# Performance work log

Measured on AMD Instinct MI355X. Metric: run time of the kernel, lower is better.

## Reference

```python
import jax, jax.numpy as jnp
import numpy as np

EPS = 1e-5


def _in_relu(y):
    # instance norm (no affine, biased var, eps=1e-5) + ReLU, y: [B,C,H,W]
    mu = jnp.mean(y, axis=(-2, -1), keepdims=True)
    var = jnp.mean((y - mu) ** 2, axis=(-2, -1), keepdims=True)
    return jax.nn.relu((y - mu) * jax.lax.rsqrt(var + EPS))


def _conv3(x, w, b):
    # x: [C,H,W], w: [O,I,3,3] -> [O,H,W]
    y = jax.lax.conv_general_dilated(x[None], w, (1, 1), ((1, 1), (1, 1)),
                                     dimension_numbers=('NCHW', 'OIHW', 'NCHW'))[0]
    return y + b[:, None, None]


def _mod_block(x, W, b, mod):
    # per-sample weight modulation: mod[n] * W, then conv+IN+relu; x: [B,C,H,W], mod: [B,O,I,3,3]
    y = jax.vmap(lambda xi, mi: _conv3(xi, mi * W, b))(x, mod)
    return _in_relu(y)


def _maxpool2(x):
    return jax.lax.reduce_window(x, -jnp.inf, jax.lax.max, (1, 1, 2, 2), (1, 1, 2, 2), 'VALID')


def _up2(x):
    B, C, H, W = x.shape
    # bilinear, half-pixel centers == PyTorch align_corners=False
    return jax.image.resize(x, (B, C, 2 * H, 2 * W), method='bilinear')


def _conv1x1(x, w, b):
    y = jax.lax.conv_general_dilated(x, w, (1, 1), 'VALID',
                                     dimension_numbers=('NCHW', 'OIHW', 'NCHW'))
    return y + b[None, :, None, None]


def setup_inputs() -> dict:
    key = jax.random.key(0)
    B, H, W = 8, 256, 256
    ks = iter(jax.random.split(key, 64))
    d = {}
    d['us_query_input'] = jax.random.normal(next(ks), (B, 1, H, W), jnp.float32)
    d['ksp_query_imgs'] = jax.random.normal(next(ks), (B, H, W, 2), jnp.float32)
    d['ksp_mask_query'] = jax.random.uniform(next(ks), (B, H, W), jnp.float32)
    down_io = [(1, 32), (32, 64), (64, 128), (128, 256)]
    up_io = [(512, 128), (256, 64), (128, 32), (64, 32)]
    for i, (ci, co) in enumerate(down_io):
        d[f'down_mod_{i}'] = jax.random.normal(next(ks), (B, co, ci, 3, 3), jnp.float32)
        d[f'W_d{i}'] = 0.05 * jax.random.normal(next(ks), (co, ci, 3, 3), jnp.float32)
        d[f'b_d{i}'] = 0.05 * jax.random.normal(next(ks), (co,), jnp.float32)
    d['latent_mod'] = jax.random.normal(next(ks), (B, 256, 256, 3, 3), jnp.float32)
    d['W_lat'] = 0.05 * jax.random.normal(next(ks), (256, 256, 3, 3), jnp.float32)
    d['b_lat'] = 0.05 * jax.random.normal(next(ks), (256,), jnp.float32)
    for i, (ci, co) in enumerate(up_io):
        d[f'up_mod_{i}'] = jax.random.normal(next(ks), (B, co, ci, 3, 3), jnp.float32)
        d[f'W_u{i}'] = 0.05 * jax.random.normal(next(ks), (co, ci, 3, 3), jnp.float32)
        d[f'b_u{i}'] = 0.05 * jax.random.normal(next(ks), (co,), jnp.float32)
    d['w_c1'] = 0.05 * jax.random.normal(next(ks), (16, 32, 1, 1), jnp.float32)
    d['b_c1'] = 0.05 * jax.random.normal(next(ks), (16,), jnp.float32)
    d['w_c2'] = 0.05 * jax.random.normal(next(ks), (1, 16, 1, 1), jnp.float32)
    d['b_c2'] = 0.05 * jax.random.normal(next(ks), (1,), jnp.float32)
    d['w_c3'] = 0.05 * jax.random.normal(next(ks), (1, 1, 1, 1), jnp.float32)
    d['b_c3'] = 0.05 * jax.random.normal(next(ks), (1,), jnp.float32)
    return d


def reference(us_query_input, ksp_query_imgs, ksp_mask_query,
              down_mod_0, down_mod_1, down_mod_2, down_mod_3,
              latent_mod, up_mod_0, up_mod_1, up_mod_2, up_mod_3,
              W_d0, b_d0, W_d1, b_d1, W_d2, b_d2, W_d3, b_d3,
              W_lat, b_lat,
              W_u0, b_u0, W_u1, b_u1, W_u2, b_u2, W_u3, b_u3,
              w_c1, b_c1, w_c2, b_c2, w_c3, b_c3):
    x0 = us_query_input
    out = x0
    skips = []
    downs = [(W_d0, b_d0, down_mod_0), (W_d1, b_d1, down_mod_1),
             (W_d2, b_d2, down_mod_2), (W_d3, b_d3, down_mod_3)]
    for Wc, bc, m in downs:
        out = _mod_block(out, Wc, bc, m)
        skips.append(out)
        out = _maxpool2(out)
    out = _mod_block(out, W_lat, b_lat, latent_mod)
    ups = [(W_u0, b_u0, up_mod_0), (W_u1, b_u1, up_mod_1),
           (W_u2, b_u2, up_mod_2), (W_u3, b_u3, up_mod_3)]
    for Wc, bc, m in ups:
        out = _up2(out)
        out = jnp.concatenate([out, skips.pop()], axis=1)
        out = _mod_block(out, Wc, bc, m)
    out = _conv1x1(_conv1x1(_conv1x1(out, w_c1, b_c1), w_c2, b_c2), w_c3, b_c3)
    out = out + x0
    # FFT data consistency
    pred = out[:, 0]                                  # [B,H,W]
    kpred = jnp.fft.fft2(pred, norm='ortho')
    ksp = ksp_query_imgs[..., 0] + 1j * ksp_query_imgs[..., 1]
    upd = ksp_mask_query * ksp + (1.0 - ksp_mask_query) * kpred
    img = jnp.fft.ifft2(upd, norm='ortho')
    return jnp.real(img)[:, None].astype(jnp.float32)   # [B,1,H,W]
```

## Files before the change

kernel.cpp:

```cpp
#include <hip/hip_runtime.h>


#define EPS_IN 1e-5f
constexpr int STST = 7936;

typedef __attribute__((ext_vector_type(8))) short short8;
typedef __attribute__((ext_vector_type(4))) short short4_t;
typedef __attribute__((ext_vector_type(4))) float f32x4;

__device__ __forceinline__ short f2bf(float f) {
    unsigned u = __float_as_uint(f);
    unsigned r = (u + 0x7fffu + ((u >> 16) & 1u)) >> 16;
    return (short)r;
}
__device__ __forceinline__ float bf2f(short s) {
    return __uint_as_float(((unsigned)(unsigned short)s) << 16);
}

__global__ void zero_f(float* __restrict__ p, int n)
{
    int i = blockIdx.x * 256 + threadIdx.x;
    if (i < n) p[i] = 0.f;
}

struct WmJobs {
    const float* W[8];
    const float* mod[8];
    short* wm[8];
    int Co[8];
    int Ci[8];
    int cum[9];
};

__global__ void make_wm_all(WmJobs j)
{
    int idx = blockIdx.x * 256 + threadIdx.x;
    if (idx >= j.cum[8]) return;
    int l = 0;
    while (idx >= j.cum[l + 1]) ++l;
    int local = idx - j.cum[l];
    const int Ci = j.Ci[l], Co = j.Co[l];
    int ci = local % Ci;
    int rem = local / Ci;
    int co = rem % Co;
    int b = rem / Co;
    const float* wp = j.W[l] + (size_t)(co * Ci + ci) * 9;
    const float* mp = j.mod[l] + ((size_t)((size_t)b * Co + co) * Ci + ci) * 9;
    short* wm = j.wm[l];
#pragma unroll
    for (int k = 0; k < 9; ++k)
        wm[(((size_t)(b * 9 + k) * Co + co) * Ci + ci)] = f2bf(wp[k] * mp[k]);
}

template <int VR, int NCOG, bool UP>
__global__ __launch_bounds__(256) void conv3x3_cl(
    const short* __restrict__ x1, int Ci1,
    const short* __restrict__ x2,
    const float2* __restrict__ st1, float invHW1,
    const short* __restrict__ wm,
    short* __restrict__ y,
    float2* __restrict__ stats,
    int Ci, int Co, int H, int W)
{
    constexpr int TH = 4 * VR, SH = TH + 2, SW = 18;
    constexpr int STN = UP ? 256 : 1;
    constexpr bool DW = (TH * 16 * NCOG * 16 * 2) <= (SH * SW * 32 * 2);
    __shared__ __align__(16) short s_x[SH][SW][32];
    __shared__ float s_red[4][4][NCOG][4][2];
    __shared__ float2 s_st1[STN];

    const int tid = threadIdx.x;
    const int lane = tid & 63, wv = tid >> 6;
    const int m = lane & 15, g = lane >> 4;

    const int b = blockIdx.x & 7;
    int r = blockIdx.x >> 3;
    const int nCoB = Co / (16 * NCOG);
    const int coblk = r % nCoB;
    const int tileId = r / nCoB;
    const int tilesx = W >> 4;
    const int tx0 = (tileId % tilesx) * 16;
    const int ty0 = (tileId / tilesx) * TH;
    const int co0 = coblk * (16 * NCOG);
    const int Ci2 = Ci - Ci1;
    const int Hs = H >> 1, Ws = W >> 1;
    const int bucket = tileId & 7;

    if (UP) {
        for (int i = tid; i < Ci1; i += 256) {
            float sx = 0.f, sy = 0.f;
#pragma unroll
            for (int k = 0; k < 8; ++k) {
                float2 v = st1[(size_t)k * STST + (size_t)b * Ci1 + i];
                sx += v.x; sy += v.y;
            }
            float mu = sx * invHW1;
            float var = sy * invHW1 - mu * mu;
            s_st1[i] = make_float2(mu, rsqrtf(var + EPS_IN));
        }
    }

    f32x4 acc[NCOG][VR];
#pragma unroll
    for (int cg = 0; cg < NCOG; ++cg)
#pragma unroll
        for (int rr = 0; rr < VR; ++rr) acc[cg][rr] = (f32x4)0.f;

    const short* wmb = wm + (size_t)b * 9 * Co * Ci;
    const short* x1b = x1 + (size_t)b * (UP ? (size_t)Hs * Ws : (size_t)H * W) * Ci1;
    const short* x2b = x2 + (size_t)b * H * W * Ci2;

    for (int ci0 = 0; ci0 < Ci; ci0 += 32) {
        __syncthreads();
        if (UP && ci0 < Ci1) {
            const int cb = ci0;
            for (int idx = tid; idx < SH * SW * 4; idx += 256) {
                int gg = idx & 3, pos = idx >> 2;
                int yy = pos / SW, xx = pos - yy * SW;
                int gy = ty0 + yy - 1, gx = tx0 + xx - 1;
                short8 v = (short8)0;
                if (gy >= 0 && gy < H && gx >= 0 && gx < W) {
                    int xk = gx >> 1, yk = gy >> 1;
                    int xo = gx & 1, yo = gy & 1;
                    int xa = xo ? xk : (xk > 0 ? xk - 1 : 0);
                    int xb = xo ? (xk + 1 < Ws ? xk + 1 : Ws - 1) : xk;
                    float wxa = xo ? 0.75f : 0.25f;
                    int ya = yo ? yk : (yk > 0 ? yk - 1 : 0);
                    int yb = yo ? (yk + 1 < Hs ? yk + 1 : Hs - 1) : yk;
                    float wya = yo ? 0.75f : 0.25f;
                    const short* ib = x1b + cb + gg * 8;
                    short8 vaa = *(const short8*)(ib + ((size_t)ya * Ws + xa) * Ci1);
                    short8 vab = *(const short8*)(ib + ((size_t)ya * Ws + xb) * Ci1);
                    short8 vba = *(const short8*)(ib + ((size_t)yb * Ws + xa) * Ci1);
                    short8 vbb = *(const short8*)(ib + ((size_t)yb * Ws + xb) * Ci1);
#pragma unroll
                    for (int e = 0; e < 8; ++e) {
                        float2 sv = s_st1[cb + gg * 8 + e];
                        float aa = fmaxf(0.f, (bf2f(vaa[e]) - sv.x) * sv.y);
                        float ab = fmaxf(0.f, (bf2f(vab[e]) - sv.x) * sv.y);
                        float ba = fmaxf(0.f, (bf2f(vba[e]) - sv.x) * sv.y);
                        float bb = fmaxf(0.f, (bf2f(vbb[e]) - sv.x) * sv.y);
                        float r0 = wxa * aa + (1.f - wxa) * ab;
                        float r1 = wxa * ba + (1.f - wxa) * bb;
                        v[e] = f2bf(wya * r0 + (1.f - wya) * r1);
                    }
                }
                *(short8*)&s_x[yy][xx][(gg ^ (xx & 3)) * 8] = v;
            }
        } else {
            const short* src; int C, cb;
            if (ci0 < Ci1) { src = x1b; C = Ci1; cb = ci0; }
            else           { src = x2b; C = Ci2; cb = ci0 - Ci1; }
            for (int idx = tid; idx < SH * SW * 4; idx += 256) {
                int gg = idx & 3, pos = idx >> 2;
                int yy = pos / SW, xx = pos - yy * SW;
                int gy = ty0 + yy - 1, gx = tx0 + xx - 1;
                short8 v = (short8)0;
                if (gy >= 0 && gy < H && gx >= 0 && gx < W)
                    v = *(const short8*)(src + ((size_t)gy * W + gx) * C + cb + gg * 8);
                *(short8*)&s_x[yy][xx][(gg ^ (xx & 3)) * 8] = v;
            }
        }
        __syncthreads();
#pragma unroll
        for (int t = 0; t < 9; ++t) {
            const int dy = t / 3, dx = t - 3 * (t / 3);
            const short* wr = wmb + ((size_t)t * Co + co0) * Ci + ci0 + g * 8;
            short8 a[NCOG];
#pragma unroll
            for (int cg = 0; cg < NCOG; ++cg)
                a[cg] = *(const short8*)(wr + (size_t)(cg * 16 + m) * Ci);
            const int xx = m + dx;
            const int sgo = (g ^ (xx & 3)) * 8;
#pragma unroll
            for (int rr = 0; rr < VR; ++rr) {
                short8 bf = *(const short8*)&s_x[wv * VR + rr + dy][xx][sgo];
#pragma unroll
                for (int cg = 0; cg < NCOG; ++cg)
                    acc[cg][rr] = __builtin_amdgcn_mfma_f32_16x16x32_bf16(a[cg], bf, acc[cg][rr], 0, 0, 0);
            }
        }
    }

    if constexpr (DW) {
        __syncthreads();
        short* sd = (short*)&s_x[0][0][0];
#pragma unroll
        for (int cg = 0; cg < NCOG; ++cg)
#pragma unroll
            for (int rr = 0; rr < VR; ++rr) {
                short4_t o;
#pragma unroll
                for (int q = 0; q < 4; ++q) o[q] = f2bf(acc[cg][rr][q]);
                *(short4_t*)&sd[((wv * VR + rr) * 16 + m) * (NCOG * 16) + cg * 16 + g * 4] = o;
            }
        __syncthreads();
        constexpr int N16 = TH * 16 * NCOG * 2;
        constexpr int CPR = NCOG * 32;
        for (int c = tid; c < N16; c += 256) {
            int row = c / CPR;
            int o16 = c % CPR;
            int p = o16 / (NCOG * 2);
            int cw = o16 % (NCOG * 2);
            short8 v = *(short8*)&sd[(row * 16 + p) * (NCOG * 16) + cw * 8];
            *(short8*)(y + (((size_t)b * H + ty0 + row) * W + tx0 + p) * Co + co0 + cw * 8) = v;
        }
    } else {
        const int ox = tx0 + m;
#pragma unroll
        for (int cg = 0; cg < NCOG; ++cg)
#pragma unroll
            for (int rr = 0; rr < VR; ++rr) {
                int oy = ty0 + wv * VR + rr;
                short4_t o;
#pragma unroll
                for (int q = 0; q < 4; ++q) o[q] = f2bf(acc[cg][rr][q]);
                *(short4_t*)(y + (((size_t)b * H + oy) * W + ox) * Co + co0 + cg * 16 + g * 4) = o;
            }
    }

#pragma unroll
    for (int cg = 0; cg < NCOG; ++cg)
#pragma unroll
        for (int q = 0; q < 4; ++q) {
            float s = 0.f, s2 = 0.f;
#pragma unroll
            for (int rr = 0; rr < VR; ++rr) { float v = acc[cg][rr][q]; s += v; s2 += v * v; }
#pragma unroll
            for (int msk = 1; msk < 16; msk <<= 1) { s += __shfl_xor(s, msk); s2 += __shfl_xor(s2, msk); }
            if (m == 0) { s_red[wv][g][cg][q][0] = s; s_red[wv][g][cg][q][1] = s2; }
        }
    __syncthreads();
    for (int i = tid; i < 16 * NCOG; i += 256) {
        int q = i & 3, gg = (i >> 2) & 3, cg = i >> 4;
        float S = 0.f, S2 = 0.f;
#pragma unroll
        for (int w = 0; w < 4; ++w) { S += s_red[w][gg][cg][q][0]; S2 += s_red[w][gg][cg][q][1]; }
        float* sp = (float*)&stats[(size_t)bucket * STST + (size_t)b * Co + co0 + i];
        atomicAdd(sp, S); atomicAdd(sp + 1, S2);
    }
}

__global__ __launch_bounds__(256) void conv_d0_cl(
    const float* __restrict__ x0, const float* __restrict__ W,
    const float* __restrict__ mod, short* __restrict__ y,
    float2* __restrict__ stats)
{
    __shared__ float s[18][18];
    __shared__ float sw[32][9];
    __shared__ float s_red[8][32][2];
    __shared__ __align__(16) short sd[16][16][32];
    const int tid = threadIdx.x;
    const int tx = tid & 15, ty = tid >> 4;
    const int tx0 = (blockIdx.x & 15) * 16, ty0 = (blockIdx.x >> 4) * 16;
    const int b = blockIdx.y;
    if (tid < 288) sw[tid / 9][tid % 9] = W[tid] * mod[b * 288 + tid];
    for (int pos = tid; pos < 18 * 18; pos += 256) {
        int yy = pos / 18, xx = pos - yy * 18;
        int gy = ty0 + yy - 1, gx = tx0 + xx - 1;
        bool inb = gy >= 0 && gy < 256 && gx >= 0 && gx < 256;
        s[yy][xx] = inb ? x0[((size_t)b << 16) + gy * 256 + gx] : 0.f;
    }
    __syncthreads();
    float v[3][3];
#pragma unroll
    for (int r = 0; r < 3; ++r)
#pragma unroll
        for (int c = 0; c < 3; ++c) v[r][c] = s[ty + r][tx + c];
    float vals[32];
#pragma unroll
    for (int co = 0; co < 32; ++co) {
        float a = 0.f;
#pragma unroll
        for (int r = 0; r < 3; ++r)
#pragma unroll
            for (int c = 0; c < 3; ++c) a = fmaf(v[r][c], sw[co][r * 3 + c], a);
        vals[co] = a;
    }
#pragma unroll
    for (int j = 0; j < 4; ++j) {
        short8 o;
#pragma unroll
        for (int e = 0; e < 8; ++e) o[e] = f2bf(vals[j * 8 + e]);
        *(short8*)&sd[ty][tx][j * 8] = o;
    }
    __syncthreads();
    for (int c = tid; c < 1024; c += 256) {
        int row = c >> 6, o = c & 63;
        short8 vv = *(short8*)&sd[row][o >> 2][(o & 3) * 8];
        *(short8*)(y + (((size_t)b * 256 + ty0 + row) * 256 + tx0 + (o >> 2)) * 32 + (o & 3) * 8) = vv;
    }
    {
        const int c = tid & 31, grp = tid >> 5;
        const short* sdf = (const short*)sd;
        float ss = 0.f, ss2 = 0.f;
#pragma unroll
        for (int p = 0; p < 32; ++p) {
            float vv = bf2f(sdf[(grp * 32 + p) * 32 + c]);
            ss += vv; ss2 += vv * vv;
        }
        s_red[grp][c][0] = ss;
        s_red[grp][c][1] = ss2;
    }
    __syncthreads();
    if (tid < 32) {
        float S = 0.f, S2 = 0.f;
#pragma unroll
        for (int g2 = 0; g2 < 8; ++g2) { S += s_red[g2][tid][0]; S2 += s_red[g2][tid][1]; }
        int bucket = blockIdx.x & 7;
        float* sp = (float*)&stats[(size_t)bucket * STST + (size_t)b * 32 + tid];
        atomicAdd(sp, S); atomicAdd(sp + 1, S2);
    }
}

__global__ __launch_bounds__(256) void maxpool_cl(
    short* __restrict__ in, const float2* __restrict__ st, float invHW,
    short* __restrict__ out, int c8s, int ws, int hs, int total8)
{
    const int C = 8 << c8s;
    __shared__ float2 sst[2048];
    for (int i = threadIdx.x; i < 8 * C; i += 256) {
        int bb = i / C, c = i % C;
        float sx = 0.f, sy = 0.f;
#pragma unroll
        for (int k = 0; k < 8; ++k) {
            float2 v = st[(size_t)k * STST + (size_t)bb * C + c];
            sx += v.x; sy += v.y;
        }
        float mu = sx * invHW;
        sst[i] = make_float2(mu, rsqrtf(sy * invHW - mu * mu + EPS_IN));
    }
    __syncthreads();
    for (int idx = blockIdx.x * 256 + threadIdx.x; idx < total8; idx += gridDim.x * 256) {
        int c8 = idx & ((1 << c8s) - 1);
        int p = idx >> c8s;
        int x = p & ((1 << ws) - 1);
        int yy = (p >> ws) & ((1 << hs) - 1);
        int b = p >> (ws + hs);
        short* ip = in + (((size_t)b * (2 << hs) + 2 * yy) * (2 << ws) + 2 * x) * C + c8 * 8;
        size_t rs = (size_t)(2 << ws) * C;
        short8 v0 = *(const short8*)ip, v1 = *(const short8*)(ip + C);
        short8 v2 = *(const short8*)(ip + rs), v3 = *(const short8*)(ip + rs + C);
        short8 o, w0, w1, w2, w3;
#pragma unroll
        for (int e = 0; e < 8; ++e) {
            float2 sv = sst[b * C + c8 * 8 + e];
            float n0 = fmaxf(0.f, (bf2f(v0[e]) - sv.x) * sv.y);
            float n1 = fmaxf(0.f, (bf2f(v1[e]) - sv.x) * sv.y);
            float n2 = fmaxf(0.f, (bf2f(v2[e]) - sv.x) * sv.y);
            float n3 = fmaxf(0.f, (bf2f(v3[e]) - sv.x) * sv.y);
            w0[e] = f2bf(n0); w1[e] = f2bf(n1); w2[e] = f2bf(n2); w3[e] = f2bf(n3);
            o[e] = f2bf(fmaxf(fmaxf(n0, n1), fmaxf(n2, n3)));
        }
        *(short8*)ip = w0;
        *(short8*)(ip + C) = w1;
        *(short8*)(ip + rs) = w2;
        *(short8*)(ip + rs + C) = w3;
        *(short8*)(out + (size_t)idx * 8) = o;
    }
}

__global__ __launch_bounds__(256) void upsample_cl(
    const short* __restrict__ in, const float2* __restrict__ st, float invHW,
    short* __restrict__ out, int c8s, int wsi, int hsi, int total8)
{
    const int C = 8 << c8s;
    const int Win = 1 << wsi, Hin = 1 << hsi;
    __shared__ float2 sst[2048];
    for (int i = threadIdx.x; i < 8 * C; i += 256) {
        int bb = i / C, c = i % C;
        float sx = 0.f, sy = 0.f;
#pragma unroll
        for (int k = 0; k < 8; ++k) {
            float2 v = st[(size_t)k * STST + (size_t)bb * C + c];
            sx += v.x; sy += v.y;
        }
        float mu = sx * invHW;
        sst[i] = make_float2(mu, rsqrtf(sy * invHW - mu * mu + EPS_IN));
    }
    __syncthreads();
    for (int idx = blockIdx.x * 256 + threadIdx.x; idx < total8; idx += gridDim.x * 256) {
        int c8 = idx & ((1 << c8s) - 1);
        int p = idx >> c8s;
        int x = p & (2 * Win - 1);
        int yy = (p >> (wsi + 1)) & (2 * Hin - 1);
        int b = p >> (wsi + 1 + hsi + 1);
        int xk = x >> 1, yk = yy >> 1;
        int xa, xb; float wxa;
        if (x & 1) { xa = xk; xb = (xk + 1 < Win) ? xk + 1 : Win - 1; wxa = 0.75f; }
        else       { xa = (xk > 0) ? xk - 1 : 0; xb = xk; wxa = 0.25f; }
        int ya, yb; float wya;
        if (yy & 1) { ya = yk; yb = (yk + 1 < Hin) ? yk + 1 : Hin - 1; wya = 0.75f; }
        else        { ya = (yk > 0) ? yk - 1 : 0; yb = yk; wya = 0.25f; }
        const short* ib = in + (size_t)b * Hin * Win * C + c8 * 8;
        short8 vaa = *(const short8*)(ib + ((size_t)ya * Win + xa) * C);
        short8 vab = *(const short8*)(ib + ((size_t)ya * Win + xb) * C);
        short8 vba = *(const short8*)(ib + ((size_t)yb * Win + xa) * C);
        short8 vbb = *(const short8*)(ib + ((size_t)yb * Win + xb) * C);
        short8 o;
#pragma unroll
        for (int e = 0; e < 8; ++e) {
            float2 sv = sst[b * C + c8 * 8 + e];
            float aa = fmaxf(0.f, (bf2f(vaa[e]) - sv.x) * sv.y);
            float ab = fmaxf(0.f, (bf2f(vab[e]) - sv.x) * sv.y);
            float ba = fmaxf(0.f, (bf2f(vba[e]) - sv.x) * sv.y);
            float bb = fmaxf(0.f, (bf2f(vbb[e]) - sv.x) * sv.y);
            float r0 = wxa * aa + (1.f - wxa) * ab;
            float r1 = wxa * ba + (1.f - wxa) * bb;
            o[e] = f2bf(wya * r0 + (1.f - wya) * r1);
        }
        *(short8*)(out + (size_t)idx * 8) = o;
    }
}

__global__ void eff1x1(const float* __restrict__ w1, const float* __restrict__ b1,
                       const float* __restrict__ w2, const float* __restrict__ b2,
                       const float* __restrict__ w3, const float* __restrict__ b3,
                       float* __restrict__ eff)
{
    int t = threadIdx.x;
    if (t < 32) {
        float s = 0.f;
        for (int k = 0; k < 16; ++k) s += w2[k] * w1[k * 32 + t];
        eff[t] = w3[0] * s;
    }
    if (t == 32) {
        float s = 0.f;
        for (int k = 0; k < 16; ++k) s += w2[k] * b1[k];
        eff[32] = w3[0] * (s + b2[0]) + b3[0];
    }
}

__device__ __forceinline__ void fft256(float2* s, int tid, float sign)
{
    __syncthreads();
#pragma unroll
    for (int t = 0; t < 4; ++t) {
        int i = tid + t * 64;
        int r = __brev(i) >> 24;
        if (r > i) { float2 tmp = s[i]; s[i] = s[r]; s[r] = tmp; }
    }
    __syncthreads();
    for (int st = 1; st <= 8; ++st) {
        int m = 1 << st, half = m >> 1;
#pragma unroll
        for (int t = 0; t < 2; ++t) {
            int k = tid + t * 64;
            int g = k >> (st - 1), j = k & (half - 1);
            int i0 = (g << st) + j, i1 = i0 + half;
            float ang = sign * 6.283185307179586f * (float)j / (float)m;
            float sn, cs;
            __sincosf(ang, &sn, &cs);
            float2 a = s[i0], b = s[i1];
            float2 tt = make_float2(b.x * cs - b.y * sn, b.x * sn + b.y * cs);
            s[i0] = make_float2(a.x + tt.x, a.y + tt.y);
            s[i1] = make_float2(a.x - tt.x, a.y - tt.y);
        }
        __syncthreads();
    }
}

__global__ __launch_bounds__(64) void final_fft_rows(
    const short* __restrict__ act, const float2* __restrict__ st, float invHW,
    const float* __restrict__ x0, const float* __restrict__ eff,
    float2* __restrict__ cplx)
{
    __shared__ float2 s[256];
    __shared__ float2 sst[32];
    __shared__ float seff[33];
    const int row = blockIdx.x, tid = threadIdx.x;
    const int b = row >> 8, yy = row & 255;
    if (tid < 32) {
        float sx = 0.f, sy = 0.f;
#pragma unroll
        for (int k = 0; k < 8; ++k) {
            float2 v = st[(size_t)k * STST + (size_t)b * 32 + tid];
            sx += v.x; sy += v.y;
        }
        float mu = sx * invHW;
        sst[tid] = make_float2(mu, rsqrtf(sy * invHW - mu * mu + EPS_IN));
    }
    if (tid < 33) seff[tid] = eff[tid];
    __syncthreads();
#pragma unroll
    for (int k = 0; k < 4; ++k) {
        int x = k * 64 + tid;
        const short8* a = (const short8*)(act + (((size_t)b * 256 + yy) * 256 + x) * 32);
        float sacc = seff[32] + x0[((size_t)b << 16) + (yy << 8) + x];
#pragma unroll
        for (int j = 0; j < 4; ++j) {
            short8 v = a[j];
#pragma unroll
            for (int e = 0; e < 8; ++e) {
                float2 sv = sst[j * 8 + e];
                sacc += seff[j * 8 + e] * fmaxf(0.f, (bf2f(v[e]) - sv.x) * sv.y);
            }
        }
        s[x] = make_float2(sacc, 0.f);
    }
    fft256(s, tid, -1.f);
    float2* o = cplx + (size_t)row * 256;
    for (int i = tid; i < 256; i += 64) o[i] = s[i];
}

__global__ __launch_bounds__(64) void fft_cols_combine(float2* __restrict__ data,
                                                       const float* __restrict__ ksp,
                                                       const float* __restrict__ mask)
{
    __shared__ float2 s[256];
    int col = blockIdx.x & 255, b = blockIdx.x >> 8;
    int tid = threadIdx.x;
    float2* base = data + (size_t)b * 65536 + col;
    for (int i = tid; i < 256; i += 64) s[i] = base[(size_t)i * 256];
    fft256(s, tid, -1.f);
    for (int i = tid; i < 256; i += 64) {
        size_t mi = ((size_t)b * 256 + i) * 256 + col;
        float m = mask[mi];
        float2 kp = s[i];
        float kr = ksp[mi * 2], ki = ksp[mi * 2 + 1];
        s[i] = make_float2(m * kr + (1.f - m) * kp.x * (1.f / 256.f),
                           m * ki + (1.f - m) * kp.y * (1.f / 256.f));
    }
    fft256(s, tid, 1.f);
    for (int i = tid; i < 256; i += 64) base[(size_t)i * 256] = s[i];
}

__global__ __launch_bounds__(64) void fft_rows_inv(const float2* __restrict__ data,
                                                   float* __restrict__ out)
{
    __shared__ float2 s[256];
    int row = blockIdx.x, tid = threadIdx.x;
    const float2* p = data + (size_t)row * 256;
    for (int i = tid; i < 256; i += 64) s[i] = p[i];
    fft256(s, tid, 1.f);
    float* o = out + (size_t)row * 256;
    for (int i = tid; i < 256; i += 64) o[i] = s[i].x * (1.f / 256.f);
}

extern "C" void kernel_launch(void* const* d_in, const int* in_sizes, int n_in,
                              void* d_out, int out_size, void* d_ws, size_t ws_size,
                              hipStream_t stream)
{
    (void)in_sizes; (void)n_in; (void)out_size; (void)ws_size;

    const float* x0 = (const float*)d_in[0];
    const float* ksp = (const float*)d_in[1];
    const float* mask = (const float*)d_in[2];
    const float* mod_d[4] = {(const float*)d_in[3], (const float*)d_in[6],
                             (const float*)d_in[9], (const float*)d_in[12]};
    const float* W_d[4] = {(const float*)d_in[4], (const float*)d_in[7],
                           (const float*)d_in[10], (const float*)d_in[13]};
    const float* mod_lat = (const float*)d_in[15];
    const float* W_lat = (const float*)d_in[16];
    const float* mod_u[4] = {(const float*)d_in[18], (const float*)d_in[21],
                             (const float*)d_in[24], (const float*)d_in[27]};
    const float* W_u[4] = {(const float*)d_in[19], (const float*)d_in[22],
                           (const float*)d_in[25], (const float*)d_in[28]};
    const float* w_c1 = (const float*)d_in[30];
    const float* b_c1 = (const float*)d_in[31];
    const float* w_c2 = (const float*)d_in[32];
    const float* b_c2 = (const float*)d_in[33];
    const float* w_c3 = (const float*)d_in[34];
    const float* b_c3 = (const float*)d_in[35];

    short* sA  = (short*)d_ws;
    short* sB  = sA + 16777216;
    short* sk0 = sB + 16777216;
    short* sk1 = sk0 + 16777216;
    short* sk2 = sk1 + 8388608;
    short* sk3 = sk2 + 4194304;
    short* wm_d1 = sk3 + 2097152;
    short* wm_d2 = wm_d1 + 147456;
    short* wm_d3 = wm_d2 + 589824;
    short* wm_lat = wm_d3 + 2359296;
    short* wm_u0 = wm_lat + 4718592;
    short* wm_u1 = wm_u0 + 4718592;
    short* wm_u2 = wm_u1 + 1179648;
    short* wm_u3 = wm_u2 + 294912;
    float2* cplx = (float2*)(wm_u3 + 147456);
    float2* stA = cplx + 524288;
    float* eff = (float*)(stA + 8 * STST);

    float2* st_d0 = stA + 0;
    float2* st_d1 = stA + 256;
    float2* st_d2 = stA + 768;
    float2* st_d3 = stA + 1792;
    float2* st_lat = stA + 3840;
    float2* st_u0 = stA + 5888;
    float2* st_u1 = stA + 6912;
    float2* st_u2 = stA + 7424;
    float2* st_u3 = stA + 7680;

    const float i64k = 1.f / 65536.f, i16k = 1.f / 16384.f, i4k = 1.f / 4096.f,
                i1k = 1.f / 1024.f, i256 = 1.f / 256.f;

    dim3 blk(256);

    zero_f<<<496, blk, 0, stream>>>((float*)stA, 8 * STST * 2);
    eff1x1<<<1, 64, 0, stream>>>(w_c1, b_c1, w_c2, b_c2, w_c3, b_c3, eff);

    WmJobs jobs;
    const float* Wl[8]  = {W_d[1], W_d[2], W_d[3], W_lat, W_u[0], W_u[1], W_u[2], W_u[3]};
    const float* Ml[8]  = {mod_d[1], mod_d[2], mod_d[3], mod_lat, mod_u[0], mod_u[1], mod_u[2], mod_u[3]};
    short* WMl[8] = {wm_d1, wm_d2, wm_d3, wm_lat, wm_u0, wm_u1, wm_u2, wm_u3};
    int Col[8] = {64, 128, 256, 256, 128, 64, 32, 32};
    int Cil[8] = {32, 64, 128, 256, 512, 256, 128, 64};
    jobs.cum[0] = 0;
    for (int l = 0; l < 8; ++l) {
        jobs.W[l] = Wl[l]; jobs.mod[l] = Ml[l]; jobs.wm[l] = WMl[l];
        jobs.Co[l] = Col[l]; jobs.Ci[l] = Cil[l];
        jobs.cum[l + 1] = jobs.cum[l] + 8 * Col[l] * Cil[l];
    }
    make_wm_all<<<(jobs.cum[8] + 255) / 256, blk, 0, stream>>>(jobs);

    conv_d0_cl<<<dim3(256, 8), blk, 0, stream>>>(x0, W_d[0], mod_d[0], sk0, st_d0);
    maxpool_cl<<<2048, blk, 0, stream>>>(sk0, st_d0, i64k, sA, 2, 7, 7, 524288);

    conv3x3_cl<4, 4, false><<<512, blk, 0, stream>>>(sA, 32, sA, stA, 0.f, wm_d1, sk1, st_d1, 32, 64, 128, 128);
    maxpool_cl<<<1024, blk, 0, stream>>>(sk1, st_d1, i16k, sA, 3, 6, 6, 262144);

    conv3x3_cl<2, 4, false><<<512, blk, 0, stream>>>(sA, 64, sA, stA, 0.f, wm_d2, sk2, st_d2, 64, 128, 64, 64);
    maxpool_cl<<<512, blk, 0, stream>>>(sk2, st_d2, i4k, sA, 4, 5, 5, 131072);

    conv3x3_cl<2, 2, false><<<512, blk, 0, stream>>>(sA, 128, sA, stA, 0.f, wm_d3, sk3, st_d3, 128, 256, 32, 32);
    maxpool_cl<<<256, blk, 0, stream>>>(sk3, st_d3, i1k, sA, 5, 4, 4, 65536);

    conv3x3_cl<2, 1, false><<<256, blk, 0, stream>>>(sA, 256, sA, stA, 0.f, wm_lat, sB, st_lat, 256, 256, 16, 16);

    upsample_cl<<<1024, blk, 0, stream>>>(sB, st_lat, i256, sA, 5, 4, 4, 262144);
    conv3x3_cl<2, 1, false><<<512, blk, 0, stream>>>(sA, 256, sk3, stA, 0.f, wm_u0, sB, st_u0, 512, 128, 32, 32);
    conv3x3_cl<2, 2, true><<<512, blk, 0, stream>>>(sB, 128, sk2, st_u0, i1k, wm_u1, sA, st_u1, 256, 64, 64, 64);
    conv3x3_cl<4, 2, true><<<512, blk, 0, stream>>>(sA, 64, sk1, st_u1, i4k, wm_u2, sB, st_u2, 128, 32, 128, 128);
    conv3x3_cl<4, 2, true><<<2048, blk, 0, stream>>>(sB, 32, sk0, st_u2, i16k, wm_u3, sA, st_u3, 64, 32, 256, 256);

    final_fft_rows<<<2048, 64, 0, stream>>>(sA, st_u3, i64k, x0, eff, cplx);

    fft_cols_combine<<<2048, 64, 0, stream>>>(cplx, ksp, mask);
    fft_rows_inv<<<2048, 64, 0, stream>>>(cplx, (float*)d_out);
}
```

Measured before the change: 471.3 us.

## Merge setup kernels, stage low-res normalized tile in LDS, batch column FFTs

Three setup launches (zeroing the stats buffer, building the effective 1x1 weights, building the modulated weights) become one kernel that branches on block index. The upsampling conv paths now load each low-resolution input tile once into shared memory with instance norm and ReLU already applied, so the bilinear gather no longer does four global loads and four normalizations per output pixel. The column FFT plus data-consistency step now processes 8 columns per 256-thread block with coalesced row loads, replacing the single-column 64-thread blocks that read with a 256-element stride. The trade is more shared memory and extra syncs in the conv, plus per-butterfly __sincosf twiddles in the new FFT.

```diff
diff --git a/kernel.cpp b/kernel.cpp
--- a/kernel.cpp
+++ b/kernel.cpp
@@ -17,39 +17,55 @@
     return __uint_as_float(((unsigned)(unsigned short)s) << 16);
 }
 
-__global__ void zero_f(float* __restrict__ p, int n)
-{
-    int i = blockIdx.x * 256 + threadIdx.x;
-    if (i < n) p[i] = 0.f;
-}
-
-struct WmJobs {
+struct SetupJobs {
     const float* W[8];
     const float* mod[8];
     short* wm[8];
     int Co[8];
     int Ci[8];
     int cum[9];
+    const float *w1, *b1, *w2, *b2, *w3, *b3;
+    float* eff;
+    float* stats;
+    int statN;
+    int wmBlocks;
 };
 
-__global__ void make_wm_all(WmJobs j)
-{
-    int idx = blockIdx.x * 256 + threadIdx.x;
-    if (idx >= j.cum[8]) return;
-    int l = 0;
-    while (idx >= j.cum[l + 1]) ++l;
-    int local = idx - j.cum[l];
-    const int Ci = j.Ci[l], Co = j.Co[l];
-    int ci = local % Ci;
-    int rem = local / Ci;
-    int co = rem % Co;
-    int b = rem / Co;
-    const float* wp = j.W[l] + (size_t)(co * Ci + ci) * 9;
-    const float* mp = j.mod[l] + ((size_t)((size_t)b * Co + co) * Ci + ci) * 9;
-    short* wm = j.wm[l];
-#pragma unroll
-    for (int k = 0; k < 9; ++k)
-        wm[(((size_t)(b * 9 + k) * Co + co) * Ci + ci)] = f2bf(wp[k] * mp[k]);
+__global__ void setup_all(SetupJobs j)
+{
+    const int bx = blockIdx.x, tid = threadIdx.x;
+    if (bx < j.wmBlocks) {
+        int idx = bx * 256 + tid;
+        if (idx >= j.cum[8]) return;
+        int l = 0;
+        while (idx >= j.cum[l + 1]) ++l;
+        int local = idx - j.cum[l];
+        const int Ci = j.Ci[l], Co = j.Co[l];
+        int ci = local % Ci;
+        int rem = local / Ci;
+        int co = rem % Co;
+        int b = rem / Co;
+        const float* wp = j.W[l] + (size_t)(co * Ci + ci) * 9;
+        const float* mp = j.mod[l] + ((size_t)((size_t)b * Co + co) * Ci + ci) * 9;
+        short* wm = j.wm[l];
+#pragma unroll
+        for (int k = 0; k < 9; ++k)
+            wm[(((size_t)(b * 9 + k) * Co + co) * Ci + ci)] = f2bf(wp[k] * mp[k]);
+    } else if (bx == j.wmBlocks) {
+        if (tid < 32) {
+            float s = 0.f;
+            for (int k = 0; k < 16; ++k) s += j.w2[k] * j.w1[k * 32 + tid];
+            j.eff[tid] = j.w3[0] * s;
+        }
+        if (tid == 32) {
+            float s = 0.f;
+            for (int k = 0; k < 16; ++k) s += j.w2[k] * j.b1[k];
+            j.eff[32] = j.w3[0] * (s + j.b2[0]) + j.b3[0];
+        }
+    } else {
+        int i = (bx - j.wmBlocks - 1) * 256 + tid;
+        if (i < j.statN) j.stats[i] = 0.f;
+    }
 }
 
 template <int VR, int NCOG, bool UP>
@@ -63,11 +79,14 @@
     int Ci, int Co, int H, int W)
 {
     constexpr int TH = 4 * VR, SH = TH + 2, SW = 18;
-    constexpr int STN = UP ? 256 : 1;
-    constexpr bool DW = (TH * 16 * NCOG * 16 * 2) <= (SH * SW * 32 * 2);
+    constexpr int STN = UP ? 128 : 1;
+    constexpr int LH = UP ? (TH / 2 + 2) : 1;
+    constexpr int LW = 10, LRW = LW * 8;
+    constexpr bool DW = (TH * 16 * NCOG * 16) <= (SH * SW * 32);
     __shared__ __align__(16) short s_x[SH][SW][32];
     __shared__ float s_red[4][4][NCOG][4][2];
     __shared__ float2 s_st1[STN];
+    __shared__ __align__(16) short s_lr[UP ? 4 : 1][LH][LRW];
 
     const int tid = threadIdx.x;
     const int lane = tid & 63, wv = tid >> 6;
@@ -114,6 +133,22 @@
         __syncthreads();
         if (UP && ci0 < Ci1) {
             const int cb = ci0;
+            const int ly0 = (ty0 >> 1) - 1, lx0 = (tx0 >> 1) - 1;
+            for (int i2 = tid; i2 < 4 * LH * LW; i2 += 256) {
+                int gg = i2 & 3, p2 = i2 >> 2;
+                int jj = p2 / LW, ii = p2 - jj * LW;
+                int sy2 = ly0 + jj; sy2 = sy2 < 0 ? 0 : (sy2 >= Hs ? Hs - 1 : sy2);
+                int sx2 = lx0 + ii; sx2 = sx2 < 0 ? 0 : (sx2 >= Ws ? Ws - 1 : sx2);
+                short8 v = *(const short8*)(x1b + ((size_t)sy2 * Ws + sx2) * Ci1 + cb + gg * 8);
+                short8 o;
+#pragma unroll
+                for (int e = 0; e < 8; ++e) {
+                    float2 sv = s_st1[cb + gg * 8 + e];
+                    o[e] = f2bf(fmaxf(0.f, (bf2f(v[e]) - sv.x) * sv.y));
+                }
+                *(short8*)&s_lr[gg][jj][ii * 8] = o;
+            }
+            __syncthreads();
             for (int idx = tid; idx < SH * SW * 4; idx += 256) {
                 int gg = idx & 3, pos = idx >> 2;
                 int yy = pos / SW, xx = pos - yy * SW;
@@ -128,20 +163,16 @@
                     int ya = yo ? yk : (yk > 0 ? yk - 1 : 0);
                     int yb = yo ? (yk + 1 < Hs ? yk + 1 : Hs - 1) : yk;
                     float wya = yo ? 0.75f : 0.25f;
-                    const short* ib = x1b + cb + gg * 8;
-                    short8 vaa = *(const short8*)(ib + ((size_t)ya * Ws + xa) * Ci1);
-                    short8 vab = *(const short8*)(ib + ((size_t)ya * Ws + xb) * Ci1);
-                    short8 vba = *(const short8*)(ib + ((size_t)yb * Ws + xa) * Ci1);
-                    short8 vbb = *(const short8*)(ib + ((size_t)yb * Ws + xb) * Ci1);
+                    int ja = ya - ly0, jb = yb - ly0;
+                    int ia = xa - lx0, ib2 = xb - lx0;
+                    short8 vaa = *(const short8*)&s_lr[gg][ja][ia * 8];
+                    short8 vab = *(const short8*)&s_lr[gg][ja][ib2 * 8];
+                    short8 vba = *(const short8*)&s_lr[gg][jb][ia * 8];
+                    short8 vbb = *(const short8*)&s_lr[gg][jb][ib2 * 8];
 #pragma unroll
                     for (int e = 0; e < 8; ++e) {
-                        float2 sv = s_st1[cb + gg * 8 + e];
-                        float aa = fmaxf(0.f, (bf2f(vaa[e]) - sv.x) * sv.y);
-                        float ab = fmaxf(0.f, (bf2f(vab[e]) - sv.x) * sv.y);
-                        float ba = fmaxf(0.f, (bf2f(vba[e]) - sv.x) * sv.y);
-                        float bb = fmaxf(0.f, (bf2f(vbb[e]) - sv.x) * sv.y);
-                        float r0 = wxa * aa + (1.f - wxa) * ab;
-                        float r1 = wxa * ba + (1.f - wxa) * bb;
+                        float r0 = wxa * bf2f(vaa[e]) + (1.f - wxa) * bf2f(vab[e]);
+                        float r1 = wxa * bf2f(vba[e]) + (1.f - wxa) * bf2f(vbb[e]);
                         v[e] = f2bf(wya * r0 + (1.f - wya) * r1);
                     }
                 }
@@ -413,24 +444,6 @@
     }
 }
 
-__global__ void eff1x1(const float* __restrict__ w1, const float* __restrict__ b1,
-                       const float* __restrict__ w2, const float* __restrict__ b2,
-                       const float* __restrict__ w3, const float* __restrict__ b3,
-                       float* __restrict__ eff)
-{
-    int t = threadIdx.x;
-    if (t < 32) {
-        float s = 0.f;
-        for (int k = 0; k < 16; ++k) s += w2[k] * w1[k * 32 + t];
-        eff[t] = w3[0] * s;
-    }
-    if (t == 32) {
-        float s = 0.f;
-        for (int k = 0; k < 16; ++k) s += w2[k] * b1[k];
-        eff[32] = w3[0] * (s + b2[0]) + b3[0];
-    }
-}
-
 __device__ __forceinline__ void fft256(float2* s, int tid, float sign)
 {
     __syncthreads();
@@ -503,26 +516,83 @@
     for (int i = tid; i < 256; i += 64) o[i] = s[i];
 }
 
-__global__ __launch_bounds__(64) void fft_cols_combine(float2* __restrict__ data,
-                                                       const float* __restrict__ ksp,
-                                                       const float* __restrict__ mask)
-{
-    __shared__ float2 s[256];
-    int col = blockIdx.x & 255, b = blockIdx.x >> 8;
-    int tid = threadIdx.x;
-    float2* base = data + (size_t)b * 65536 + col;
-    for (int i = tid; i < 256; i += 64) s[i] = base[(size_t)i * 256];
-    fft256(s, tid, -1.f);
-    for (int i = tid; i < 256; i += 64) {
-        size_t mi = ((size_t)b * 256 + i) * 256 + col;
-        float m = mask[mi];
-        float2 kp = s[i];
+__global__ __launch_bounds__(256) void fft_cols_combine8(
+    float2* __restrict__ data, const float* __restrict__ ksp,
+    const float* __restrict__ mask)
+{
+    __shared__ float2 s2[8][260];
+    const int tid = threadIdx.x;
+    const int b = blockIdx.x >> 5;
+    const int col0 = (blockIdx.x & 31) * 8;
+    float2* base = data + (size_t)b * 65536 + col0;
+    for (int idx = tid; idx < 2048; idx += 256) {
+        int row = idx >> 3, c = idx & 7;
+        s2[c][row] = base[row * 256 + c];
+    }
+    __syncthreads();
+    const int c = tid >> 5, lt = tid & 31;
+#pragma unroll
+    for (int t = 0; t < 8; ++t) {
+        int i = lt + t * 32;
+        int r = __brev(i) >> 24;
+        if (r > i) { float2 tmp = s2[c][i]; s2[c][i] = s2[c][r]; s2[c][r] = tmp; }
+    }
+    __syncthreads();
+    for (int st = 1; st <= 8; ++st) {
+        int m = 1 << st, half = m >> 1;
+#pragma unroll
+        for (int t = 0; t < 4; ++t) {
+            int k = lt + t * 32;
+            int g = k >> (st - 1), j = k & (half - 1);
+            int i0 = (g << st) + j, i1 = i0 + half;
+            float ang = -6.283185307179586f * (float)j / (float)m;
+            float sn, cs;
+            __sincosf(ang, &sn, &cs);
+            float2 a = s2[c][i0], bb = s2[c][i1];
+            float2 tt = make_float2(bb.x * cs - bb.y * sn, bb.x * sn + bb.y * cs);
+            s2[c][i0] = make_float2(a.x + tt.x, a.y + tt.y);
+            s2[c][i1] = make_float2(a.x - tt.x, a.y - tt.y);
+        }
+        __syncthreads();
+    }
+    for (int idx = tid; idx < 2048; idx += 256) {
+        int row = idx >> 3, cc = idx & 7;
+        size_t mi = ((size_t)b * 256 + row) * 256 + col0 + cc;
+        float mval = mask[mi];
+        float2 kp = s2[cc][row];
         float kr = ksp[mi * 2], ki = ksp[mi * 2 + 1];
-        s[i] = make_float2(m * kr + (1.f - m) * kp.x * (1.f / 256.f),
-                           m * ki + (1.f - m) * kp.y * (1.f / 256.f));
-    }
-    fft256(s, tid, 1.f);
-    for (int i = tid; i < 256; i += 64) base[(size_t)i * 256] = s[i];
+        s2[cc][row] = make_float2(mval * kr + (1.f - mval) * kp.x * (1.f / 256.f),
+                                  mval * ki + (1.f - mval) * kp.y * (1.f / 256.f));
+    }
+    __syncthreads();
+#pragma unroll
+    for (int t = 0; t < 8; ++t) {
+        int i = lt + t * 32;
+        int r = __brev(i) >> 24;
+        if (r > i) { float2 tmp = s2[c][i]; s2[c][i] = s2[c][r]; s2[c][r] = tmp; }
+    }
+    __syncthreads();
+    for (int st = 1; st <= 8; ++st) {
+        int m = 1 << st, half = m >> 1;
+#pragma unroll
+        for (int t = 0; t < 4; ++t) {
+            int k = lt + t * 32;
+            int g = k >> (st - 1), j = k & (half - 1);
+            int i0 = (g << st) + j, i1 = i0 + half;
+            float ang = 6.283185307179586f * (float)j / (float)m;
+            float sn, cs;
+            __sincosf(ang, &sn, &cs);
+            float2 a = s2[c][i0], bb = s2[c][i1];
+            float2 tt = make_float2(bb.x * cs - bb.y * sn, bb.x * sn + bb.y * cs);
+            s2[c][i0] = make_float2(a.x + tt.x, a.y + tt.y);
+            s2[c][i1] = make_float2(a.x - tt.x, a.y - tt.y);
+        }
+        __syncthreads();
+    }
+    for (int idx = tid; idx < 2048; idx += 256) {
+        int row = idx >> 3, cc = idx & 7;
+        base[row * 256 + cc] = s2[cc][row];
+    }
 }
 
 __global__ __launch_bounds__(64) void fft_rows_inv(const float2* __restrict__ data,
@@ -596,10 +666,7 @@
 
     dim3 blk(256);
 
-    zero_f<<<496, blk, 0, stream>>>((float*)stA, 8 * STST * 2);
-    eff1x1<<<1, 64, 0, stream>>>(w_c1, b_c1, w_c2, b_c2, w_c3, b_c3, eff);
-
-    WmJobs jobs;
+    SetupJobs jobs;
     const float* Wl[8]  = {W_d[1], W_d[2], W_d[3], W_lat, W_u[0], W_u[1], W_u[2], W_u[3]};
     const float* Ml[8]  = {mod_d[1], mod_d[2], mod_d[3], mod_lat, mod_u[0], mod_u[1], mod_u[2], mod_u[3]};
     short* WMl[8] = {wm_d1, wm_d2, wm_d3, wm_lat, wm_u0, wm_u1, wm_u2, wm_u3};
@@ -611,7 +678,14 @@
         jobs.Co[l] = Col[l]; jobs.Ci[l] = Cil[l];
         jobs.cum[l + 1] = jobs.cum[l] + 8 * Col[l] * Cil[l];
     }
-    make_wm_all<<<(jobs.cum[8] + 255) / 256, blk, 0, stream>>>(jobs);
+    jobs.w1 = w_c1; jobs.b1 = b_c1; jobs.w2 = w_c2; jobs.b2 = b_c2;
+    jobs.w3 = w_c3; jobs.b3 = b_c3;
+    jobs.eff = eff;
+    jobs.stats = (float*)stA;
+    jobs.statN = 8 * STST * 2;
+    jobs.wmBlocks = (jobs.cum[8] + 255) / 256;
+    int setupGrid = jobs.wmBlocks + 1 + (jobs.statN + 255) / 256;
+    setup_all<<<setupGrid, blk, 0, stream>>>(jobs);
 
     conv_d0_cl<<<dim3(256, 8), blk, 0, stream>>>(x0, W_d[0], mod_d[0], sk0, st_d0);
     maxpool_cl<<<2048, blk, 0, stream>>>(sk0, st_d0, i64k, sA, 2, 7, 7, 524288);
@@ -635,6 +709,6 @@
 
     final_fft_rows<<<2048, 64, 0, stream>>>(sA, st_u3, i64k, x0, eff, cplx);
 
-    fft_cols_combine<<<2048, 64, 0, stream>>>(cplx, ksp, mask);
+    fft_cols_combine8<<<256, blk, 0, stream>>>(cplx, ksp, mask);
     fft_rows_inv<<<2048, 64, 0, stream>>>(cplx, (float*)d_out);
 }
```

After: 444.9 us. -5.6%, faster.
